# Kernel optimization log

Measured on AMD Instinct MI355X. Metric: run time of the kernel, lower is better.

The kernel has to match this reference:

```python
import jax, jax.numpy as jnp
import numpy as np
from jax import lax

B, N, D = 8, 65536, 64

def setup_inputs() -> dict:
    key = jax.random.key(0)
    k1, k2, k3 = jax.random.split(key, 3)
    return {
        "x": jax.random.normal(k1, (B, D), dtype=jnp.float32),
        "z": jax.random.normal(k2, (B, D), dtype=jnp.float32),
        "means": jax.random.normal(k3, (B, N, D), dtype=jnp.float32),
        "sigma": jnp.float32(1.0),
        "iterations": 10,
    }

def reference(x, z, means, sigma, iterations):
    # x is unused by the original module's forward (kept for signature parity)
    inv_temp = -0.5 / (sigma ** 2)

    def step(z_c, _):
        # squared distance ||z - mean_i||^2 per memory slot: [B, N]
        d2 = jnp.sum((z_c[:, None, :] - means) ** 2, axis=-1)
        w = jax.nn.softmax(inv_temp * d2, axis=1)          # [B, N]
        z_new = jnp.einsum('bn,bnd->bd', w, means)          # [B, D]
        return z_new, None

    z_out, _ = lax.scan(step, z, None, length=iterations)
    return z_out
```

## Files before the change

### kernel.cpp

```cpp
#include <hip/hip_runtime.h>
#include <hip/hip_fp16.h>
#include <math.h>

#define B_    8
#define N_    65536
#define D_    64
#define ITERS 10

#define NBLK  256
#define TPB   256
#define CHUNK (N_ / NBLK)

#define GROUPS 16
#define KSTATES 4
#define JITER (CHUNK / (GROUPS * KSTATES))

#define LPR2  8
#define GRP2  (TPB / LPR2)
#define KS2   2
#define JIT2  (CHUNK / (GRP2 * KS2))

template <int WRITE_H>
__global__ __launch_bounds__(TPB) void gmm_f32(
    const float* __restrict__ z,
    const float* __restrict__ means,
    const float* __restrict__ sigma_p,
    float* __restrict__ pm,
    float* __restrict__ pl,
    float* __restrict__ pacc,
    __half* __restrict__ mh)
{
    const int blk  = blockIdx.x;
    const int b    = blockIdx.y;
    const int tid  = threadIdx.x;
    const int grp  = tid >> 4;
    const int lane = tid & 15;

    const float sigma = sigma_p[0];
    const float c2 = (-0.5f / (sigma * sigma)) * 1.44269504088896340736f;

    const float4 zv = *(const float4*)(z + b * D_ + lane * 4);

    const size_t rowidx = (size_t)b * N_ + (size_t)blk * CHUNK + grp;
    const float4* p = (const float4*)(means + rowidx * D_) + lane;
    uint2* hp = (uint2*)mh + rowidx * 16 + lane;

    float  m[KSTATES], l[KSTATES];
    float4 acc[KSTATES];
#pragma unroll
    for (int k = 0; k < KSTATES; ++k) {
        m[k] = -INFINITY; l[k] = 0.0f;
        acc[k] = make_float4(0.f, 0.f, 0.f, 0.f);
    }

    float4 cur[KSTATES];
#pragma unroll
    for (int k = 0; k < KSTATES; ++k) cur[k] = p[k * 256];

#pragma unroll
    for (int j = 0; j < JITER; ++j) {
        float4 nxt[KSTATES];
        if (j + 1 < JITER) {
#pragma unroll
            for (int k = 0; k < KSTATES; ++k) nxt[k] = p[(j + 1) * 1024 + k * 256];
        }
#pragma unroll
        for (int k = 0; k < KSTATES; ++k) {
            const float4 mv = cur[k];
            if (WRITE_H) {
                const __half2 h01 = __float22half2_rn(make_float2(mv.x, mv.y));
                const __half2 h23 = __float22half2_rn(make_float2(mv.z, mv.w));
                uint2 u;
                u.x = *reinterpret_cast<const unsigned int*>(&h01);
                u.y = *reinterpret_cast<const unsigned int*>(&h23);
                hp[j * 1024 + k * 256] = u;
            }
            const float dx = zv.x - mv.x;
            const float dy = zv.y - mv.y;
            const float dz = zv.z - mv.z;
            const float dw = zv.w - mv.w;
            float s = dx * dx + dy * dy + dz * dz + dw * dw;
            s += __shfl_xor(s, 1);
            s += __shfl_xor(s, 2);
            s += __shfl_xor(s, 4);
            s += __shfl_xor(s, 8);

            const float t  = c2 * s;
            const float mn = fmaxf(m[k], t);
            const float sc = exp2f(m[k] - mn);
            const float w  = exp2f(t - mn);
            l[k]  = l[k] * sc + w;
            acc[k].x = acc[k].x * sc + w * mv.x;
            acc[k].y = acc[k].y * sc + w * mv.y;
            acc[k].z = acc[k].z * sc + w * mv.z;
            acc[k].w = acc[k].w * sc + w * mv.w;
            m[k] = mn;
        }
#pragma unroll
        for (int k = 0; k < KSTATES; ++k) cur[k] = nxt[k];
    }

    float M = fmaxf(fmaxf(m[0], m[1]), fmaxf(m[2], m[3]));
    float L = 0.0f;
    float ax = 0.f, ay = 0.f, az = 0.f, aw = 0.f;
#pragma unroll
    for (int k = 0; k < KSTATES; ++k) {
        const float wk = exp2f(m[k] - M);
        L  += wk * l[k];
        ax += wk * acc[k].x;
        ay += wk * acc[k].y;
        az += wk * acc[k].z;
        aw += wk * acc[k].w;
    }

    __shared__ float s_m[GROUPS];
    __shared__ float s_l[GROUPS];
    __shared__ __align__(16) float s_acc[GROUPS][D_];

    if (lane == 0) { s_m[grp] = M; s_l[grp] = L; }
    *(float4*)&s_acc[grp][lane * 4] = make_float4(ax, ay, az, aw);
    __syncthreads();

    if (tid < D_) {
        float Mb = -INFINITY;
#pragma unroll
        for (int g = 0; g < GROUPS; ++g) Mb = fmaxf(Mb, s_m[g]);
        float Lb = 0.0f;
        float a  = 0.0f;
#pragma unroll
        for (int g = 0; g < GROUPS; ++g) {
            const float wg = exp2f(s_m[g] - Mb);
            Lb += wg * s_l[g];
            a  += wg * s_acc[g][tid];
        }
        const int pidx = b * NBLK + blk;
        pacc[(size_t)pidx * D_ + tid] = a;
        if (tid == 0) { pm[pidx] = Mb; pl[pidx] = Lb; }
    }
}

__global__ __launch_bounds__(TPB) void gmm_f16(
    const float* __restrict__ z,
    const __half* __restrict__ mh,
    const float* __restrict__ sigma_p,
    float* __restrict__ pm,
    float* __restrict__ pl,
    float* __restrict__ pacc)
{
    const int blk  = blockIdx.x;
    const int b    = blockIdx.y;
    const int tid  = threadIdx.x;
    const int grp  = tid >> 3;
    const int lane = tid & 7;

    const float sigma = sigma_p[0];
    const float c2 = (-0.5f / (sigma * sigma)) * 1.44269504088896340736f;

    const float4* zp = (const float4*)(z + b * D_) + lane * 2;
    const float4 z0v = zp[0];
    const float4 z1v = zp[1];

    const size_t rowidx = (size_t)b * N_ + (size_t)blk * CHUNK + grp;
    const uint4* p = (const uint4*)mh + rowidx * 8 + lane;

    float  m[KS2], l[KS2];
    float4 a0[KS2], a1[KS2];
#pragma unroll
    for (int k = 0; k < KS2; ++k) {
        m[k] = -INFINITY; l[k] = 0.0f;
        a0[k] = make_float4(0.f, 0.f, 0.f, 0.f);
        a1[k] = make_float4(0.f, 0.f, 0.f, 0.f);
    }

    uint4 cur[KS2];
#pragma unroll
    for (int k = 0; k < KS2; ++k) cur[k] = p[k * 256];

#pragma unroll
    for (int j = 0; j < JIT2; ++j) {
        uint4 nxt[KS2];
        if (j + 1 < JIT2) {
#pragma unroll
            for (int k = 0; k < KS2; ++k) nxt[k] = p[(j + 1) * 512 + k * 256];
        }
#pragma unroll
        for (int k = 0; k < KS2; ++k) {
            const __half2* h = reinterpret_cast<const __half2*>(&cur[k]);
            const float2 f0 = __half22float2(h[0]);
            const float2 f1 = __half22float2(h[1]);
            const float2 f2 = __half22float2(h[2]);
            const float2 f3 = __half22float2(h[3]);
            const float4 mv0 = make_float4(f0.x, f0.y, f1.x, f1.y);
            const float4 mv1 = make_float4(f2.x, f2.y, f3.x, f3.y);

            const float d0 = z0v.x - mv0.x;
            const float d1 = z0v.y - mv0.y;
            const float d2 = z0v.z - mv0.z;
            const float d3 = z0v.w - mv0.w;
            const float d4 = z1v.x - mv1.x;
            const float d5 = z1v.y - mv1.y;
            const float d6 = z1v.z - mv1.z;
            const float d7 = z1v.w - mv1.w;
            float s = d0 * d0 + d1 * d1 + d2 * d2 + d3 * d3
                    + d4 * d4 + d5 * d5 + d6 * d6 + d7 * d7;
            s += __shfl_xor(s, 1);
            s += __shfl_xor(s, 2);
            s += __shfl_xor(s, 4);

            const float t  = c2 * s;
            const float mn = fmaxf(m[k], t);
            const float sc = exp2f(m[k] - mn);
            const float w  = exp2f(t - mn);
            l[k] = l[k] * sc + w;
            a0[k].x = a0[k].x * sc + w * mv0.x;
            a0[k].y = a0[k].y * sc + w * mv0.y;
            a0[k].z = a0[k].z * sc + w * mv0.z;
            a0[k].w = a0[k].w * sc + w * mv0.w;
            a1[k].x = a1[k].x * sc + w * mv1.x;
            a1[k].y = a1[k].y * sc + w * mv1.y;
            a1[k].z = a1[k].z * sc + w * mv1.z;
            a1[k].w = a1[k].w * sc + w * mv1.w;
            m[k] = mn;
        }
#pragma unroll
        for (int k = 0; k < KS2; ++k) cur[k] = nxt[k];
    }

    const float M = fmaxf(m[0], m[1]);
    float L = 0.0f;
    float4 A0 = make_float4(0.f, 0.f, 0.f, 0.f);
    float4 A1 = make_float4(0.f, 0.f, 0.f, 0.f);
#pragma unroll
    for (int k = 0; k < KS2; ++k) {
        const float wk = exp2f(m[k] - M);
        L += wk * l[k];
        A0.x += wk * a0[k].x;  A0.y += wk * a0[k].y;
        A0.z += wk * a0[k].z;  A0.w += wk * a0[k].w;
        A1.x += wk * a1[k].x;  A1.y += wk * a1[k].y;
        A1.z += wk * a1[k].z;  A1.w += wk * a1[k].w;
    }

    __shared__ float s_m[GRP2];
    __shared__ float s_l[GRP2];
    __shared__ __align__(16) float s_acc[GRP2][D_];

    if (lane == 0) { s_m[grp] = M; s_l[grp] = L; }
    *(float4*)&s_acc[grp][lane * 8]     = A0;
    *(float4*)&s_acc[grp][lane * 8 + 4] = A1;
    __syncthreads();

    if (tid < D_) {
        float Mb = -INFINITY;
#pragma unroll
        for (int g = 0; g < GRP2; ++g) Mb = fmaxf(Mb, s_m[g]);
        float Lb = 0.0f;
        float a  = 0.0f;
#pragma unroll
        for (int g = 0; g < GRP2; ++g) {
            const float wg = exp2f(s_m[g] - Mb);
            Lb += wg * s_l[g];
            a  += wg * s_acc[g][tid];
        }
        const int pidx = b * NBLK + blk;
        pacc[(size_t)pidx * D_ + tid] = a;
        if (tid == 0) { pm[pidx] = Mb; pl[pidx] = Lb; }
    }
}

__global__ __launch_bounds__(256) void gmm_phase2(
    const float* __restrict__ pm,
    const float* __restrict__ pl,
    const float* __restrict__ pacc,
    float* __restrict__ z_out,
    float* __restrict__ final_out)
{
    const int b = blockIdx.x;
    const int t = threadIdx.x;
    const int d = t & 63;
    const int q = t >> 6;

    __shared__ float s_red[256];
    __shared__ float s_L[4];

    s_red[t] = pm[b * NBLK + t];
    __syncthreads();
    for (int s = 128; s > 0; s >>= 1) {
        if (t < s) s_red[t] = fmaxf(s_red[t], s_red[t + s]);
        __syncthreads();
    }
    const float M = s_red[0];
    __syncthreads();

    float L = 0.0f, A = 0.0f;
    for (int k = 0; k < 64; ++k) {
        const int pi = b * NBLK + q * 64 + k;
        const float wg = exp2f(pm[pi] - M);
        L += wg * pl[pi];
        A += wg * pacc[(size_t)pi * D_ + d];
    }

    s_red[q * 64 + d] = A;
    if (d == 0) s_L[q] = L;
    __syncthreads();

    if (t < D_) {
        float As = s_red[t] + s_red[64 + t] + s_red[128 + t] + s_red[192 + t];
        float Ls = s_L[0] + s_L[1] + s_L[2] + s_L[3];
        const float zv = As / Ls;
        z_out[b * D_ + t] = zv;
        if (final_out) final_out[b * D_ + t] = zv;
    }
}

extern "C" void kernel_launch(void* const* d_in, const int* in_sizes, int n_in,
                              void* d_out, int out_size, void* d_ws, size_t ws_size,
                              hipStream_t stream)
{
    const float* z0    = (const float*)d_in[1];
    const float* means = (const float*)d_in[2];
    const float* sigma = (const float*)d_in[3];
    float* out = (float*)d_out;

    float* ws = (float*)d_ws;

    const size_t MH_FLOATS = (size_t)B_ * N_ * D_ / 2;
    const size_t NEED = (MH_FLOATS + 2048 + 2048 + (size_t)B_ * NBLK * D_ + 512) * 4;

    if (ws_size >= NEED) {
        __half* mh  = (__half*)ws;
        float* pm   = ws + MH_FLOATS;
        float* pl   = pm + B_ * NBLK;
        float* pacc = pl + B_ * NBLK;
        float* zbuf = pacc + (size_t)B_ * NBLK * D_;

        for (int it = 0; it < ITERS; ++it) {
            const float* zin = (it == 0) ? z0 : zbuf;
            if (it == 0) {
                gmm_f32<1><<<dim3(NBLK, B_), TPB, 0, stream>>>(
                    zin, means, sigma, pm, pl, pacc, mh);
            } else {
                gmm_f16<<<dim3(NBLK, B_), TPB, 0, stream>>>(
                    zin, mh, sigma, pm, pl, pacc);
            }
            gmm_phase2<<<B_, 256, 0, stream>>>(pm, pl, pacc, zbuf,
                                               (it == ITERS - 1) ? out : nullptr);
        }
    } else {
        float* pm   = ws;
        float* pl   = pm + B_ * NBLK;
        float* pacc = pl + B_ * NBLK;
        float* zbuf = pacc + (size_t)B_ * NBLK * D_;

        for (int it = 0; it < ITERS; ++it) {
            const float* zin = (it == 0) ? z0 : zbuf;
            gmm_f32<0><<<dim3(NBLK, B_), TPB, 0, stream>>>(
                zin, means, sigma, pm, pl, pacc, nullptr);
            gmm_phase2<<<B_, 256, 0, stream>>>(pm, pl, pacc, zbuf,
                                               (it == ITERS - 1) ? out : nullptr);
        }
    }
}
```

Before: 384.1 us.

## Replace online softmax with fixed stabilizer from previous iteration's max

The half-precision pass no longer keeps a running max with rescaling. It subtracts the global per-batch max from the previous iteration as a fixed offset, which removes one exp2 and the rescale multiplies for every element. It also still tracks the new max so it can be passed to the next iteration. Because all partials now share the same offset, the block-level and phase-2 merges become plain sums. The risk is overflow or underflow if the log-weight max drifts far between iterations.

```diff
diff --git a/kernel.cpp b/kernel.cpp
--- a/kernel.cpp
+++ b/kernel.cpp
@@ -139,10 +139,11 @@
     }
 }
 
-__global__ __launch_bounds__(TPB) void gmm_f16(
+__global__ __launch_bounds__(TPB) void gmm_nr(
     const float* __restrict__ z,
     const __half* __restrict__ mh,
     const float* __restrict__ sigma_p,
+    const float* __restrict__ Mg,
     float* __restrict__ pm,
     float* __restrict__ pl,
     float* __restrict__ pacc)
@@ -155,6 +156,7 @@
 
     const float sigma = sigma_p[0];
     const float c2 = (-0.5f / (sigma * sigma)) * 1.44269504088896340736f;
+    const float negM = -Mg[b];
 
     const float4* zp = (const float4*)(z + b * D_) + lane * 2;
     const float4 z0v = zp[0];
@@ -163,11 +165,11 @@
     const size_t rowidx = (size_t)b * N_ + (size_t)blk * CHUNK + grp;
     const uint4* p = (const uint4*)mh + rowidx * 8 + lane;
 
-    float  m[KS2], l[KS2];
+    float  l[KS2], bm[KS2];
     float4 a0[KS2], a1[KS2];
 #pragma unroll
     for (int k = 0; k < KS2; ++k) {
-        m[k] = -INFINITY; l[k] = 0.0f;
+        l[k] = 0.0f; bm[k] = -INFINITY;
         a0[k] = make_float4(0.f, 0.f, 0.f, 0.f);
         a1[k] = make_float4(0.f, 0.f, 0.f, 0.f);
     }
@@ -207,72 +209,60 @@
             s += __shfl_xor(s, 2);
             s += __shfl_xor(s, 4);
 
-            const float t  = c2 * s;
-            const float mn = fmaxf(m[k], t);
-            const float sc = exp2f(m[k] - mn);
-            const float w  = exp2f(t - mn);
-            l[k] = l[k] * sc + w;
-            a0[k].x = a0[k].x * sc + w * mv0.x;
-            a0[k].y = a0[k].y * sc + w * mv0.y;
-            a0[k].z = a0[k].z * sc + w * mv0.z;
-            a0[k].w = a0[k].w * sc + w * mv0.w;
-            a1[k].x = a1[k].x * sc + w * mv1.x;
-            a1[k].y = a1[k].y * sc + w * mv1.y;
-            a1[k].z = a1[k].z * sc + w * mv1.z;
-            a1[k].w = a1[k].w * sc + w * mv1.w;
-            m[k] = mn;
+            const float tm = fmaf(c2, s, negM);
+            const float w  = exp2f(tm);
+            bm[k] = fmaxf(bm[k], tm);
+            l[k] += w;
+            a0[k].x = fmaf(w, mv0.x, a0[k].x);
+            a0[k].y = fmaf(w, mv0.y, a0[k].y);
+            a0[k].z = fmaf(w, mv0.z, a0[k].z);
+            a0[k].w = fmaf(w, mv0.w, a0[k].w);
+            a1[k].x = fmaf(w, mv1.x, a1[k].x);
+            a1[k].y = fmaf(w, mv1.y, a1[k].y);
+            a1[k].z = fmaf(w, mv1.z, a1[k].z);
+            a1[k].w = fmaf(w, mv1.w, a1[k].w);
         }
 #pragma unroll
         for (int k = 0; k < KS2; ++k) cur[k] = nxt[k];
     }
 
-    const float M = fmaxf(m[0], m[1]);
-    float L = 0.0f;
-    float4 A0 = make_float4(0.f, 0.f, 0.f, 0.f);
-    float4 A1 = make_float4(0.f, 0.f, 0.f, 0.f);
-#pragma unroll
-    for (int k = 0; k < KS2; ++k) {
-        const float wk = exp2f(m[k] - M);
-        L += wk * l[k];
-        A0.x += wk * a0[k].x;  A0.y += wk * a0[k].y;
-        A0.z += wk * a0[k].z;  A0.w += wk * a0[k].w;
-        A1.x += wk * a1[k].x;  A1.y += wk * a1[k].y;
-        A1.z += wk * a1[k].z;  A1.w += wk * a1[k].w;
-    }
+    const float Lg = l[0] + l[1];
+    const float bmg = fmaxf(bm[0], bm[1]);
+    float4 A0, A1;
+    A0.x = a0[0].x + a0[1].x;  A0.y = a0[0].y + a0[1].y;
+    A0.z = a0[0].z + a0[1].z;  A0.w = a0[0].w + a0[1].w;
+    A1.x = a1[0].x + a1[1].x;  A1.y = a1[0].y + a1[1].y;
+    A1.z = a1[0].z + a1[1].z;  A1.w = a1[0].w + a1[1].w;
 
     __shared__ float s_m[GRP2];
     __shared__ float s_l[GRP2];
     __shared__ __align__(16) float s_acc[GRP2][D_];
 
-    if (lane == 0) { s_m[grp] = M; s_l[grp] = L; }
+    if (lane == 0) { s_m[grp] = bmg; s_l[grp] = Lg; }
     *(float4*)&s_acc[grp][lane * 8]     = A0;
     *(float4*)&s_acc[grp][lane * 8 + 4] = A1;
     __syncthreads();
 
     if (tid < D_) {
-        float Mb = -INFINITY;
-#pragma unroll
-        for (int g = 0; g < GRP2; ++g) Mb = fmaxf(Mb, s_m[g]);
-        float Lb = 0.0f;
-        float a  = 0.0f;
+        float a = 0.0f, Lb = 0.0f, mb = -INFINITY;
 #pragma unroll
         for (int g = 0; g < GRP2; ++g) {
-            const float wg = exp2f(s_m[g] - Mb);
-            Lb += wg * s_l[g];
-            a  += wg * s_acc[g][tid];
+            a  += s_acc[g][tid];
+            Lb += s_l[g];
+            mb  = fmaxf(mb, s_m[g]);
         }
         const int pidx = b * NBLK + blk;
         pacc[(size_t)pidx * D_ + tid] = a;
-        if (tid == 0) { pm[pidx] = Mb; pl[pidx] = Lb; }
-    }
-}
-
-__global__ __launch_bounds__(256) void gmm_phase2(
+        if (tid == 0) { pm[pidx] = mb - negM; pl[pidx] = Lb; }
+    }
+}
+
+__global__ __launch_bounds__(256) void gmm_phase2_init(
     const float* __restrict__ pm,
     const float* __restrict__ pl,
     const float* __restrict__ pacc,
     float* __restrict__ z_out,
-    float* __restrict__ final_out)
+    float* __restrict__ Mout)
 {
     const int b = blockIdx.x;
     const int t = threadIdx.x;
@@ -304,12 +294,58 @@
     __syncthreads();
 
     if (t < D_) {
-        float As = s_red[t] + s_red[64 + t] + s_red[128 + t] + s_red[192 + t];
-        float Ls = s_L[0] + s_L[1] + s_L[2] + s_L[3];
+        const float As = s_red[t] + s_red[64 + t] + s_red[128 + t] + s_red[192 + t];
+        const float Ls = s_L[0] + s_L[1] + s_L[2] + s_L[3];
+        z_out[b * D_ + t] = As / Ls;
+    }
+    if (t == 0) Mout[b] = M;
+}
+
+__global__ __launch_bounds__(256) void gmm_phase2_lite(
+    const float* __restrict__ pm,
+    const float* __restrict__ pl,
+    const float* __restrict__ pacc,
+    float* __restrict__ z_out,
+    float* __restrict__ Mout,
+    float* __restrict__ final_out)
+{
+    const int b = blockIdx.x;
+    const int t = threadIdx.x;
+    const int d = t & 63;
+    const int q = t >> 6;
+    const int base = b * NBLK;
+
+    __shared__ float s_red[256];
+    __shared__ float s_L[4];
+
+    s_red[t] = pm[base + t];
+    __syncthreads();
+    for (int s = 128; s > 0; s >>= 1) {
+        if (t < s) s_red[t] = fmaxf(s_red[t], s_red[t + s]);
+        __syncthreads();
+    }
+    const float M = s_red[0];
+    __syncthreads();
+
+    float L = 0.0f, A = 0.0f;
+    for (int k = 0; k < 64; ++k) {
+        const int pi = base + q * 64 + k;
+        L += pl[pi];
+        A += pacc[(size_t)pi * D_ + d];
+    }
+
+    s_red[q * 64 + d] = A;
+    if (d == 0) s_L[q] = L;
+    __syncthreads();
+
+    if (t < D_) {
+        const float As = s_red[t] + s_red[64 + t] + s_red[128 + t] + s_red[192 + t];
+        const float Ls = s_L[0] + s_L[1] + s_L[2] + s_L[3];
         const float zv = As / Ls;
         z_out[b * D_ + t] = zv;
         if (final_out) final_out[b * D_ + t] = zv;
     }
+    if (t == 0) Mout[b] = M;
 }
 
 extern "C" void kernel_launch(void* const* d_in, const int* in_sizes, int n_in,
@@ -324,7 +360,8 @@
     float* ws = (float*)d_ws;
 
     const size_t MH_FLOATS = (size_t)B_ * N_ * D_ / 2;
-    const size_t NEED = (MH_FLOATS + 2048 + 2048 + (size_t)B_ * NBLK * D_ + 512) * 4;
+    const size_t NEED = (MH_FLOATS + 2048 + 2048
+                         + (size_t)B_ * NBLK * D_ + 512 + 64) * 4;
 
     if (ws_size >= NEED) {
         __half* mh  = (__half*)ws;
@@ -332,31 +369,31 @@
         float* pl   = pm + B_ * NBLK;
         float* pacc = pl + B_ * NBLK;
         float* zbuf = pacc + (size_t)B_ * NBLK * D_;
-
-        for (int it = 0; it < ITERS; ++it) {
-            const float* zin = (it == 0) ? z0 : zbuf;
-            if (it == 0) {
-                gmm_f32<1><<<dim3(NBLK, B_), TPB, 0, stream>>>(
-                    zin, means, sigma, pm, pl, pacc, mh);
-            } else {
-                gmm_f16<<<dim3(NBLK, B_), TPB, 0, stream>>>(
-                    zin, mh, sigma, pm, pl, pacc);
-            }
-            gmm_phase2<<<B_, 256, 0, stream>>>(pm, pl, pacc, zbuf,
-                                               (it == ITERS - 1) ? out : nullptr);
+        float* Mg   = zbuf + B_ * D_;
+
+        gmm_f32<1><<<dim3(NBLK, B_), TPB, 0, stream>>>(
+            z0, means, sigma, pm, pl, pacc, mh);
+        gmm_phase2_init<<<B_, 256, 0, stream>>>(pm, pl, pacc, zbuf, Mg);
+
+        for (int it = 1; it < ITERS; ++it) {
+            gmm_nr<<<dim3(NBLK, B_), TPB, 0, stream>>>(
+                zbuf, mh, sigma, Mg, pm, pl, pacc);
+            gmm_phase2_lite<<<B_, 256, 0, stream>>>(
+                pm, pl, pacc, zbuf, Mg, (it == ITERS - 1) ? out : nullptr);
         }
     } else {
         float* pm   = ws;
         float* pl   = pm + B_ * NBLK;
         float* pacc = pl + B_ * NBLK;
         float* zbuf = pacc + (size_t)B_ * NBLK * D_;
+        float* Mg   = zbuf + B_ * D_;
 
         for (int it = 0; it < ITERS; ++it) {
             const float* zin = (it == 0) ? z0 : zbuf;
             gmm_f32<0><<<dim3(NBLK, B_), TPB, 0, stream>>>(
                 zin, means, sigma, pm, pl, pacc, nullptr);
-            gmm_phase2<<<B_, 256, 0, stream>>>(pm, pl, pacc, zbuf,
-                                               (it == ITERS - 1) ? out : nullptr);
-        }
-    }
-}
+            gmm_phase2_init<<<B_, 256, 0, stream>>>(
+                pm, pl, pacc, (it == ITERS - 1) ? out : zbuf, Mg);
+        }
+    }
+}
```

Measured after the change: 366.8 us. -4.5%, faster.
